# Optimization experiments

Hardware: AMD Instinct MI355X
Metric: run time of the kernel (lower is better)

## Reference

```python
import jax, jax.numpy as jnp
import numpy as np

DICE_W, BCE_W = 1.0, 1.0
BBOX_W = 0.025
L1_W, GIOU_W = 1.0, 1.0  # assumed BoxLoss weighting: loss = l1.sum(-1) + (1 - giou)


def _xywh_to_xyxy(b):
    cx, cy, w, h = b[..., 0], b[..., 1], b[..., 2], b[..., 3]
    return jnp.stack([cx - w / 2, cy - h / 2, cx + w / 2, cy + h / 2], axis=-1)


def _xyxy_to_xywh(b):
    x1, y1, x2, y2 = b[..., 0], b[..., 1], b[..., 2], b[..., 3]
    return jnp.stack([(x1 + x2) / 2, (y1 + y2) / 2, x2 - x1, y2 - y1], axis=-1)


def _giou(a, b):
    # a, b: [N,4] xyxy, paired GIoU
    ix1 = jnp.maximum(a[:, 0], b[:, 0]); iy1 = jnp.maximum(a[:, 1], b[:, 1])
    ix2 = jnp.minimum(a[:, 2], b[:, 2]); iy2 = jnp.minimum(a[:, 3], b[:, 3])
    inter = jnp.clip(ix2 - ix1, 0) * jnp.clip(iy2 - iy1, 0)
    area_a = jnp.clip(a[:, 2] - a[:, 0], 0) * jnp.clip(a[:, 3] - a[:, 1], 0)
    area_b = jnp.clip(b[:, 2] - b[:, 0], 0) * jnp.clip(b[:, 3] - b[:, 1], 0)
    union = area_a + area_b - inter
    iou = inter / jnp.maximum(union, 1e-6)
    cx1 = jnp.minimum(a[:, 0], b[:, 0]); cy1 = jnp.minimum(a[:, 1], b[:, 1])
    cx2 = jnp.maximum(a[:, 2], b[:, 2]); cy2 = jnp.maximum(a[:, 3], b[:, 3])
    c = jnp.clip(cx2 - cx1, 0) * jnp.clip(cy2 - cy1, 0)
    return iou - (c - union) / jnp.maximum(c, 1e-6)


def _box_loss_per_sample(pred_xywh, tgt_xywh):
    l1 = jnp.abs(pred_xywh - tgt_xywh).sum(-1)
    g = 1.0 - _giou(_xywh_to_xyxy(pred_xywh), _xywh_to_xyxy(tgt_xywh))
    return L1_W * l1 + GIOU_W * g


def _forward(pred_mask, pred_bbox, gt_bbox_rand, target_mask, img_h, img_w):
    B = pred_mask.shape[0]
    H, W = img_h, img_w
    tgt = target_mask.astype(pred_mask.dtype)          # [B,H,W] binary
    logits = pred_mask[:, 0]                           # [B,H,W]
    probs = jax.nn.sigmoid(logits)

    # ---- seg_loss: dice + bce (both mean-reduced) ----
    p = probs.reshape(B, -1); t = tgt.reshape(B, -1)
    dice = 1.0 - (2.0 * (p * t).sum(1) + 1.0) / (p.sum(1) + t.sum(1) + 1.0)
    x = logits.reshape(B, -1)
    bce = jnp.maximum(x, 0) - x * t + jnp.log1p(jnp.exp(-jnp.abs(x)))
    loss_mask = DICE_W * dice.mean() + BCE_W * bce.mean()

    # ---- bbox_loss: gt x1y1x2y2 (pixels) -> normalized cxcywh ----
    gx1 = gt_bbox_rand[:, 0] * (0.45 * W); gy1 = gt_bbox_rand[:, 1] * (0.45 * H)
    gx2 = gx1 + 1.0 + gt_bbox_rand[:, 2] * (0.5 * W)
    gy2 = gy1 + 1.0 + gt_bbox_rand[:, 3] * (0.5 * H)
    gt_xyxy = jnp.stack([gx1, gy1, gx2, gy2], axis=-1)
    # original divides by img_size [H,W] repeated -> [H,W,H,W] (square imgs)
    norm_div = jnp.asarray([H, W, H, W], dtype=pred_bbox.dtype)
    gt_norm = _xyxy_to_xywh(gt_xyxy) / norm_div
    loss_det = _box_loss_per_sample(pred_bbox, gt_norm).mean() * BBOX_W

    # ---- boxseg_iouloss2 (vectorized over the per-batch python loop) ----
    box_xyxy = _xywh_to_xyxy(pred_bbox)                # normalized xyxy
    scale = jnp.asarray([W, H, W, H], dtype=pred_bbox.dtype)
    pix = (box_xyxy * scale).astype(jnp.int32)         # trunc like .to(int)
    x1p = jnp.clip(pix[:, 0], 0, W); x2p = jnp.clip(pix[:, 2], 0, W)
    y1p = jnp.clip(pix[:, 1], 0, H); y2p = jnp.clip(pix[:, 3], 0, H)
    seg_bin = (probs > 0.5).astype(pred_mask.dtype)    # S2Bthr == B2Sthr == 0.5
    xs = jnp.arange(W); ys = jnp.arange(H)
    in_x = (xs[None, :] >= x1p[:, None]) & (xs[None, :] < x2p[:, None])  # [B,W]
    in_y = (ys[None, :] >= y1p[:, None]) & (ys[None, :] < y2p[:, None])  # [B,H]
    inside = in_y[:, :, None] & in_x[:, None, :]                          # [B,H,W]
    inter = (seg_bin * inside).sum((1, 2))
    area = seg_bin.sum((1, 2))
    s2b_iou = jnp.where(area > 0, inter / jnp.maximum(area, 1.0), 0.0)
    loss_s2b = (1.0 - s2b_iou).mean()

    # get_maskouterbox: per-sample min/max of coords where mask is on
    mb = seg_bin.astype(bool)
    x1o = jnp.min(jnp.where(mb, xs[None, None, :], W), axis=(1, 2))
    y1o = jnp.min(jnp.where(mb, ys[None, :, None], H), axis=(1, 2))
    x2o = jnp.max(jnp.where(mb, xs[None, None, :], -1), axis=(1, 2))
    y2o = jnp.max(jnp.where(mb, ys[None, :, None], -1), axis=(1, 2))
    present = (area > 0)[:, None]
    outer = jnp.stack([x1o, y1o, x2o, y2o], axis=-1).astype(pred_bbox.dtype)
    outer = jnp.where(present, outer, 0.0) / scale
    loss_b2s = _box_loss_per_sample(_xyxy_to_xywh(outer), _xyxy_to_xywh(box_xyxy)).mean()

    return loss_mask + loss_det + loss_s2b + loss_b2s


def setup_inputs() -> dict:
    key = jax.random.key(0)
    k1, k2, k3, k4 = jax.random.split(key, 4)
    B, H, W = 64, 512, 512
    return {
        "pred_mask": jax.random.normal(k1, (B, 1, H, W), dtype=jnp.float32),
        "pred_bbox": jax.random.uniform(k2, (B, 4), dtype=jnp.float32),
        "gt_bbox_rand": jax.random.uniform(k3, (B, 4), dtype=jnp.float32),
        "target_mask": jax.random.randint(k4, (B, H, W), 0, 2, dtype=jnp.int32),
        "img_h": H,
        "img_w": W,
    }


def reference(pred_mask, pred_bbox, gt_bbox_rand, target_mask, img_h, img_w):
    return _forward(pred_mask, pred_bbox, gt_bbox_rand, target_mask, img_h, img_w)
```

## Files before the change

### kernel.cpp

```cpp
#include <hip/hip_runtime.h>
#include <math.h>


#define TPB 256

__device__ inline float box_loss_xywh(const float pb[4], const float tb[4]) {
    float l1 = fabsf(pb[0] - tb[0]) + fabsf(pb[1] - tb[1]) +
               fabsf(pb[2] - tb[2]) + fabsf(pb[3] - tb[3]);
    float ax1 = pb[0] - 0.5f * pb[2], ay1 = pb[1] - 0.5f * pb[3];
    float ax2 = pb[0] + 0.5f * pb[2], ay2 = pb[1] + 0.5f * pb[3];
    float bx1 = tb[0] - 0.5f * tb[2], by1 = tb[1] - 0.5f * tb[3];
    float bx2 = tb[0] + 0.5f * tb[2], by2 = tb[1] + 0.5f * tb[3];

    float ix1 = fmaxf(ax1, bx1), iy1 = fmaxf(ay1, by1);
    float ix2 = fminf(ax2, bx2), iy2 = fminf(ay2, by2);
    float inter  = fmaxf(ix2 - ix1, 0.f) * fmaxf(iy2 - iy1, 0.f);
    float area_a = fmaxf(ax2 - ax1, 0.f) * fmaxf(ay2 - ay1, 0.f);
    float area_b = fmaxf(bx2 - bx1, 0.f) * fmaxf(by2 - by1, 0.f);
    float uni = area_a + area_b - inter;
    float iou = inter / fmaxf(uni, 1e-6f);
    float cx1 = fminf(ax1, bx1), cy1 = fminf(ay1, by1);
    float cx2 = fmaxf(ax2, bx2), cy2 = fmaxf(ay2, by2);
    float c = fmaxf(cx2 - cx1, 0.f) * fmaxf(cy2 - cy1, 0.f);
    float giou = iou - (c - uni) / fmaxf(c, 1e-6f);
    return l1 + (1.0f - giou);
}

struct Acc {
    float s_pt, s_p, s_bce;
    int c_t, c_area, c_inter;
    unsigned rmask, colmask;
};

__device__ __forceinline__ void proc4(const float4 xv, const int4 tv,
                                      int yloc, int ybase, int by1, int by2,
                                      int inx0, int inx1, int inx2, int inx3,
                                      Acc& a)
{
    float xs[4] = {xv.x, xv.y, xv.z, xv.w};
    int   ts[4] = {tv.x, tv.y, tv.z, tv.w};
    int pos[4];
    #pragma unroll
    for (int j = 0; j < 4; ++j) {
        float xl = xs[j];
        bool  t  = ts[j] != 0;
        float e  = __expf(-fabsf(xl));
        float r  = __builtin_amdgcn_rcpf(1.f + e);
        float p  = (xl >= 0.f) ? r : e * r;
        a.s_bce += fmaxf(xl, 0.f) - (t ? xl : 0.f) - __logf(r);
        a.s_p   += p;
        a.s_pt  += t ? p : 0.f;
        a.c_t   += ts[j];
        pos[j] = xl > 0.f;
    }
    int anyp = pos[0] | pos[1] | pos[2] | pos[3];
    a.c_area  += pos[0] + pos[1] + pos[2] + pos[3];
    a.colmask |= (unsigned)(pos[0] | (pos[1] << 1) | (pos[2] << 2) | (pos[3] << 3));
    a.rmask   |= (unsigned)anyp << yloc;
    const int y = ybase + yloc;
    const int inrow = (y >= by1) & (y < by2);
    a.c_inter += inrow ? ((pos[0] & inx0) + (pos[1] & inx1) +
                          (pos[2] & inx2) + (pos[3] & inx3)) : 0;
}

__global__ __launch_bounds__(TPB, 8)
void uh_reduce(const float* __restrict__ pred_mask,
               const int*   __restrict__ target_mask,
               const float* __restrict__ pred_bbox,
               const int*   __restrict__ pH, const int* __restrict__ pW,
               float* __restrict__ wf, int* __restrict__ wi,
               int HW, int N)
{
    const int b      = blockIdx.y;
    const int chunk  = blockIdx.x;
    const int nchunk = gridDim.x;
    const int W = *pW;
    const int H = *pH;

    float c0 = pred_bbox[b * 4 + 0], c1 = pred_bbox[b * 4 + 1];
    float c2 = pred_bbox[b * 4 + 2], c3 = pred_bbox[b * 4 + 3];
    const int bx1 = min(max((int)((c0 - 0.5f * c2) * (float)W), 0), W);
    const int by1 = min(max((int)((c1 - 0.5f * c3) * (float)H), 0), H);
    const int bx2 = min(max((int)((c0 + 0.5f * c2) * (float)W), 0), W);
    const int by2 = min(max((int)((c1 + 0.5f * c3) * (float)H), 0), H);

    const int chunk_px = HW / nchunk;
    const int rows     = chunk_px / W;
    const int tpr      = W >> 2;
    const int rpi      = TPB / tpr;
    const int iters    = rows / rpi;
    const int rowoff   = threadIdx.x / tpr;
    const int cx       = (threadIdx.x - rowoff * tpr) << 2;
    const int ybase    = chunk * rows;

    const int inx0 = (cx + 0 >= bx1) & (cx + 0 < bx2);
    const int inx1 = (cx + 1 >= bx1) & (cx + 1 < bx2);
    const int inx2 = (cx + 2 >= bx1) & (cx + 2 < bx2);
    const int inx3 = (cx + 3 >= bx1) & (cx + 3 < bx2);

    const long boff = (long)b * HW + (long)(ybase + rowoff) * W + cx;
    const float* pp = pred_mask + boff;
    const int*   tp = target_mask + boff;
    const int    stride = rpi * W;

    Acc a = {0.f, 0.f, 0.f, 0, 0, 0, 0u, 0u};
    int yloc = rowoff;

    const int npairs = iters >> 1;
    float4 xa0 = *(const float4*)pp;
    int4   ta0 = *(const int4*)tp;
    float4 xa1 = *(const float4*)(pp + stride);
    int4   ta1 = *(const int4*)(tp + stride);
    pp += 2 * stride; tp += 2 * stride;

    for (int g = 0; g < npairs - 1; ++g) {
        float4 xb0 = *(const float4*)pp;
        int4   tb0 = *(const int4*)tp;
        float4 xb1 = *(const float4*)(pp + stride);
        int4   tb1 = *(const int4*)(tp + stride);
        pp += 2 * stride; tp += 2 * stride;

        proc4(xa0, ta0, yloc,       ybase, by1, by2, inx0, inx1, inx2, inx3, a);
        proc4(xa1, ta1, yloc + rpi, ybase, by1, by2, inx0, inx1, inx2, inx3, a);
        yloc += 2 * rpi;

        xa0 = xb0; ta0 = tb0; xa1 = xb1; ta1 = tb1;
    }
    proc4(xa0, ta0, yloc,       ybase, by1, by2, inx0, inx1, inx2, inx3, a);
    proc4(xa1, ta1, yloc + rpi, ybase, by1, by2, inx0, inx1, inx2, inx3, a);

    int xmn = W, xmx = -1, ymn = H, ymx = -1;
    if (a.colmask) {
        xmn = cx + (__ffs(a.colmask) - 1);
        xmx = cx + (31 - __clz(a.colmask));
    }
    if (a.rmask) {
        ymn = ybase + (__ffs(a.rmask) - 1);
        ymx = ybase + (31 - __clz(a.rmask));
    }

    float s_pt = a.s_pt, s_p = a.s_p, s_bce = a.s_bce;
    int c_t = a.c_t, c_area = a.c_area, c_inter = a.c_inter;
    #pragma unroll
    for (int o = 32; o; o >>= 1) {
        s_pt  += __shfl_down(s_pt,  o, 64);
        s_p   += __shfl_down(s_p,   o, 64);
        s_bce += __shfl_down(s_bce, o, 64);
        c_t    += __shfl_down(c_t,    o, 64);
        c_area += __shfl_down(c_area, o, 64);
        c_inter+= __shfl_down(c_inter,o, 64);
        xmn = min(xmn, __shfl_down(xmn, o, 64));
        ymn = min(ymn, __shfl_down(ymn, o, 64));
        xmx = max(xmx, __shfl_down(xmx, o, 64));
        ymx = max(ymx, __shfl_down(ymx, o, 64));
    }

    __shared__ float smf[3][4];
    __shared__ int   smi[7][4];
    const int wid = threadIdx.x >> 6;
    if ((threadIdx.x & 63) == 0) {
        smf[0][wid] = s_pt;  smf[1][wid] = s_p;  smf[2][wid] = s_bce;
        smi[0][wid] = c_t;   smi[1][wid] = c_area; smi[2][wid] = c_inter;
        smi[3][wid] = xmn;   smi[4][wid] = ymn;
        smi[5][wid] = xmx;   smi[6][wid] = ymx;
    }
    __syncthreads();
    if (threadIdx.x == 0) {
        float a0 = 0.f, a1 = 0.f, a2 = 0.f;
        int i0 = 0, i1 = 0, i2 = 0;
        int m3 = W, m4 = H, m5 = -1, m6 = -1;
        #pragma unroll
        for (int w = 0; w < 4; ++w) {
            a0 += smf[0][w]; a1 += smf[1][w]; a2 += smf[2][w];
            i0 += smi[0][w]; i1 += smi[1][w]; i2 += smi[2][w];
            m3 = min(m3, smi[3][w]); m4 = min(m4, smi[4][w]);
            m5 = max(m5, smi[5][w]); m6 = max(m6, smi[6][w]);
        }
        const int idx = b * nchunk + chunk;
        wf[0 * N + idx] = a0; wf[1 * N + idx] = a1; wf[2 * N + idx] = a2;
        wi[0 * N + idx] = i0; wi[1 * N + idx] = i1; wi[2 * N + idx] = i2;
        wi[3 * N + idx] = m3; wi[4 * N + idx] = m4;
        wi[5 * N + idx] = m5; wi[6 * N + idx] = m6;
    }
}

__global__ __launch_bounds__(TPB)
void uh_final(const float* __restrict__ pred_bbox,
              const float* __restrict__ gt_bbox,
              const int* __restrict__ pH, const int* __restrict__ pW,
              const float* __restrict__ wf, const int* __restrict__ wi,
              int B, int HW, int nchunk, float* __restrict__ out)
{
    const int W = *pW, H = *pH;
    const int N = B * nchunk;
    const int tid = threadIdx.x;
    const int b   = tid >> 2;
    const int q   = tid & 3;

    float v = 0.f;
    if (b < B) {
        float s_pt = 0.f, s_p = 0.f, s_bce = 0.f;
        int c_t = 0, c_area = 0, c_inter = 0;
        int xmn = W, ymn = H, xmx = -1, ymx = -1;
        for (int c = q; c < nchunk; c += 4) {
            const int idx = b * nchunk + c;
            s_pt  += wf[0 * N + idx];
            s_p   += wf[1 * N + idx];
            s_bce += wf[2 * N + idx];
            c_t    += wi[0 * N + idx];
            c_area += wi[1 * N + idx];
            c_inter+= wi[2 * N + idx];
            xmn = min(xmn, wi[3 * N + idx]); ymn = min(ymn, wi[4 * N + idx]);
            xmx = max(xmx, wi[5 * N + idx]); ymx = max(ymx, wi[6 * N + idx]);
        }
        #pragma unroll
        for (int o = 1; o < 4; o <<= 1) {
            s_pt  += __shfl_xor(s_pt,  o, 64);
            s_p   += __shfl_xor(s_p,   o, 64);
            s_bce += __shfl_xor(s_bce, o, 64);
            c_t    += __shfl_xor(c_t,    o, 64);
            c_area += __shfl_xor(c_area, o, 64);
            c_inter+= __shfl_xor(c_inter,o, 64);
            xmn = min(xmn, __shfl_xor(xmn, o, 64));
            ymn = min(ymn, __shfl_xor(ymn, o, 64));
            xmx = max(xmx, __shfl_xor(xmx, o, 64));
            ymx = max(ymx, __shfl_xor(ymx, o, 64));
        }

        if (q == 0) {
            float dice = 1.f - (2.f * s_pt + 1.f) / (s_p + (float)c_t + 1.f);

            float pb[4] = {pred_bbox[b*4+0], pred_bbox[b*4+1],
                           pred_bbox[b*4+2], pred_bbox[b*4+3]};
            float g0 = gt_bbox[b*4+0], g1 = gt_bbox[b*4+1];
            float g2 = gt_bbox[b*4+2], g3 = gt_bbox[b*4+3];
            float gx1 = g0 * (0.45f * (float)W);
            float gy1 = g1 * (0.45f * (float)H);
            float gx2 = gx1 + 1.0f + g2 * (0.5f * (float)W);
            float gy2 = gy1 + 1.0f + g3 * (0.5f * (float)H);
            float gt[4] = { ((gx1 + gx2) * 0.5f) / (float)H,
                            ((gy1 + gy2) * 0.5f) / (float)W,
                            (gx2 - gx1) / (float)H,
                            (gy2 - gy1) / (float)W };
            float det = 0.025f * box_loss_xywh(pb, gt);

            float iou_s2b = (c_area > 0)
                              ? (float)c_inter / fmaxf((float)c_area, 1.f) : 0.f;
            float s2b = 1.f - iou_s2b;

            float ox1, oy1, ox2, oy2;
            if (c_area > 0) {
                ox1 = (float)xmn; oy1 = (float)ymn;
                ox2 = (float)xmx; oy2 = (float)ymx;
            } else {
                ox1 = oy1 = ox2 = oy2 = 0.f;
            }
            ox1 /= (float)W; ox2 /= (float)W;
            oy1 /= (float)H; oy2 /= (float)H;
            float ow[4] = { (ox1 + ox2) * 0.5f, (oy1 + oy2) * 0.5f,
                            ox2 - ox1, oy2 - oy1 };
            float px1 = pb[0] - 0.5f * pb[2], py1 = pb[1] - 0.5f * pb[3];
            float px2 = pb[0] + 0.5f * pb[2], py2 = pb[1] + 0.5f * pb[3];
            float pw[4] = { (px1 + px2) * 0.5f, (py1 + py2) * 0.5f,
                            px2 - px1, py2 - py1 };
            float b2s = box_loss_xywh(ow, pw);

            v = dice + s_bce / (float)HW + det + s2b + b2s;
        }
    }

    #pragma unroll
    for (int o = 32; o; o >>= 1) v += __shfl_down(v, o, 64);
    __shared__ float sv[4];
    if ((tid & 63) == 0) sv[tid >> 6] = v;
    __syncthreads();
    if (tid == 0) out[0] = (sv[0] + sv[1] + sv[2] + sv[3]) / (float)B;
}

extern "C" void kernel_launch(void* const* d_in, const int* in_sizes, int n_in,
                              void* d_out, int out_size, void* d_ws, size_t ws_size,
                              hipStream_t stream) {
    const float* pred_mask   = (const float*)d_in[0];
    const float* pred_bbox   = (const float*)d_in[1];
    const float* gt_bbox     = (const float*)d_in[2];
    const int*   target_mask = (const int*)d_in[3];
    const int*   pH          = (const int*)d_in[4];
    const int*   pW          = (const int*)d_in[5];
    float* out = (float*)d_out;

    const int B  = in_sizes[1] / 4;
    const int HW = in_sizes[0] / B;

    int bps = 32;
    if ((size_t)10 * sizeof(int) * B * bps > ws_size) bps = 16;
    const int N = B * bps;

    float* wf = (float*)d_ws;
    int*   wi = (int*)d_ws + (size_t)3 * N;

    dim3 grid(bps, B);
    uh_reduce<<<grid, TPB, 0, stream>>>(pred_mask, target_mask, pred_bbox,
                                        pH, pW, wf, wi, HW, N);
    uh_final<<<1, TPB, 0, stream>>>(pred_bbox, gt_bbox, pH, pW, wf, wi,
                                    B, HW, bps, out);
}
```

Before: 159.5 us.

## Process eight columns per thread with four-row batches and cheaper BCE math

Each thread now covers 8 contiguous columns instead of 4 and loads four rows per iteration (16 vector loads in flight) in place of the software-pipelined pair loop. The BCE term is split into a relu accumulator plus a log2 sum scaled once at the end, and sigmoid uses 1-r instead of e*r. Column and row masks are built as bitmasks reduced with popcount, and the row mask now indexes iteration number rather than the local row. The launch-bounds occupancy hint is dropped, which may raise register use and lower occupancy. The intent is more memory-level parallelism and fewer ALU ops per pixel.

```diff
diff --git a/kernel.cpp b/kernel.cpp
--- a/kernel.cpp
+++ b/kernel.cpp
@@ -26,44 +26,7 @@
     return l1 + (1.0f - giou);
 }
 
-struct Acc {
-    float s_pt, s_p, s_bce;
-    int c_t, c_area, c_inter;
-    unsigned rmask, colmask;
-};
-
-__device__ __forceinline__ void proc4(const float4 xv, const int4 tv,
-                                      int yloc, int ybase, int by1, int by2,
-                                      int inx0, int inx1, int inx2, int inx3,
-                                      Acc& a)
-{
-    float xs[4] = {xv.x, xv.y, xv.z, xv.w};
-    int   ts[4] = {tv.x, tv.y, tv.z, tv.w};
-    int pos[4];
-    #pragma unroll
-    for (int j = 0; j < 4; ++j) {
-        float xl = xs[j];
-        bool  t  = ts[j] != 0;
-        float e  = __expf(-fabsf(xl));
-        float r  = __builtin_amdgcn_rcpf(1.f + e);
-        float p  = (xl >= 0.f) ? r : e * r;
-        a.s_bce += fmaxf(xl, 0.f) - (t ? xl : 0.f) - __logf(r);
-        a.s_p   += p;
-        a.s_pt  += t ? p : 0.f;
-        a.c_t   += ts[j];
-        pos[j] = xl > 0.f;
-    }
-    int anyp = pos[0] | pos[1] | pos[2] | pos[3];
-    a.c_area  += pos[0] + pos[1] + pos[2] + pos[3];
-    a.colmask |= (unsigned)(pos[0] | (pos[1] << 1) | (pos[2] << 2) | (pos[3] << 3));
-    a.rmask   |= (unsigned)anyp << yloc;
-    const int y = ybase + yloc;
-    const int inrow = (y >= by1) & (y < by2);
-    a.c_inter += inrow ? ((pos[0] & inx0) + (pos[1] & inx1) +
-                          (pos[2] & inx2) + (pos[3] & inx3)) : 0;
-}
-
-__global__ __launch_bounds__(TPB, 8)
+__global__ __launch_bounds__(TPB)
 void uh_reduce(const float* __restrict__ pred_mask,
                const int*   __restrict__ target_mask,
                const float* __restrict__ pred_bbox,
@@ -86,61 +49,93 @@
 
     const int chunk_px = HW / nchunk;
     const int rows     = chunk_px / W;
-    const int tpr      = W >> 2;
+    const int tpr      = W >> 3;
     const int rpi      = TPB / tpr;
     const int iters    = rows / rpi;
     const int rowoff   = threadIdx.x / tpr;
-    const int cx       = (threadIdx.x - rowoff * tpr) << 2;
+    const int cx       = (threadIdx.x - rowoff * tpr) << 3;
     const int ybase    = chunk * rows;
 
-    const int inx0 = (cx + 0 >= bx1) & (cx + 0 < bx2);
-    const int inx1 = (cx + 1 >= bx1) & (cx + 1 < bx2);
-    const int inx2 = (cx + 2 >= bx1) & (cx + 2 < bx2);
-    const int inx3 = (cx + 3 >= bx1) & (cx + 3 < bx2);
+    unsigned inxmask = 0;
+    #pragma unroll
+    for (int j = 0; j < 8; ++j)
+        inxmask |= (unsigned)((cx + j >= bx1) & (cx + j < bx2)) << j;
 
     const long boff = (long)b * HW + (long)(ybase + rowoff) * W + cx;
     const float* pp = pred_mask + boff;
     const int*   tp = target_mask + boff;
     const int    stride = rpi * W;
 
-    Acc a = {0.f, 0.f, 0.f, 0, 0, 0, 0u, 0u};
-    int yloc = rowoff;
-
-    const int npairs = iters >> 1;
-    float4 xa0 = *(const float4*)pp;
-    int4   ta0 = *(const int4*)tp;
-    float4 xa1 = *(const float4*)(pp + stride);
-    int4   ta1 = *(const int4*)(tp + stride);
-    pp += 2 * stride; tp += 2 * stride;
-
-    for (int g = 0; g < npairs - 1; ++g) {
-        float4 xb0 = *(const float4*)pp;
-        int4   tb0 = *(const int4*)tp;
-        float4 xb1 = *(const float4*)(pp + stride);
-        int4   tb1 = *(const int4*)(tp + stride);
-        pp += 2 * stride; tp += 2 * stride;
-
-        proc4(xa0, ta0, yloc,       ybase, by1, by2, inx0, inx1, inx2, inx3, a);
-        proc4(xa1, ta1, yloc + rpi, ybase, by1, by2, inx0, inx1, inx2, inx3, a);
-        yloc += 2 * rpi;
-
-        xa0 = xb0; ta0 = tb0; xa1 = xb1; ta1 = tb1;
-    }
-    proc4(xa0, ta0, yloc,       ybase, by1, by2, inx0, inx1, inx2, inx3, a);
-    proc4(xa1, ta1, yloc + rpi, ybase, by1, by2, inx0, inx1, inx2, inx3, a);
+    float s_pt = 0.f, s_p = 0.f, slg2 = 0.f, s_relu = 0.f;
+    int c_t = 0, c_area = 0, c_inter = 0;
+    unsigned rmask = 0, colmask = 0;
+
+    for (int gb = 0; gb < iters; gb += 4) {
+        float4 xa0 = *(const float4*)(pp);
+        float4 xb0 = *(const float4*)(pp + 4);
+        int4   ta0 = *(const int4*)(tp);
+        int4   tb0 = *(const int4*)(tp + 4);
+        float4 xa1 = *(const float4*)(pp + stride);
+        float4 xb1 = *(const float4*)(pp + stride + 4);
+        int4   ta1 = *(const int4*)(tp + stride);
+        int4   tb1 = *(const int4*)(tp + stride + 4);
+        float4 xa2 = *(const float4*)(pp + 2 * stride);
+        float4 xb2 = *(const float4*)(pp + 2 * stride + 4);
+        int4   ta2 = *(const int4*)(tp + 2 * stride);
+        int4   tb2 = *(const int4*)(tp + 2 * stride + 4);
+        float4 xa3 = *(const float4*)(pp + 3 * stride);
+        float4 xb3 = *(const float4*)(pp + 3 * stride + 4);
+        int4   ta3 = *(const int4*)(tp + 3 * stride);
+        int4   tb3 = *(const int4*)(tp + 3 * stride + 4);
+        pp += 4 * stride; tp += 4 * stride;
+
+        #define PROC_ROW(G, XA, XB, TA, TB)                                   \
+        {                                                                     \
+            const float xs[8] = {XA.x, XA.y, XA.z, XA.w,                      \
+                                 XB.x, XB.y, XB.z, XB.w};                     \
+            const int   ts[8] = {TA.x, TA.y, TA.z, TA.w,                      \
+                                 TB.x, TB.y, TB.z, TB.w};                     \
+            unsigned m8 = 0;                                                  \
+            _Pragma("unroll")                                                 \
+            for (int j = 0; j < 8; ++j) {                                     \
+                float xl = xs[j];                                             \
+                bool  t  = ts[j] != 0;                                        \
+                float e  = __expf(-fabsf(xl));           \
+                float r  = __builtin_amdgcn_rcpf(1.f + e);                    \
+                slg2    += __log2f(r);                  \
+                float p  = (xl >= 0.f) ? r : 1.f - r;                         \
+                s_p     += p;                                                 \
+                s_pt    += t ? p : 0.f;                                       \
+                s_relu  += fmaxf(t ? -xl : xl, 0.f);                          \
+                c_t     += ts[j];                                             \
+                m8      |= (unsigned)(xl > 0.f) << j;                         \
+            }                                                                 \
+            c_area  += __popc(m8);                                            \
+            const int y = ybase + rowoff + (G) * rpi;                         \
+            c_inter += ((y >= by1) & (y < by2)) ? __popc(m8 & inxmask) : 0;   \
+            colmask |= m8;                                                    \
+            rmask   |= (m8 ? 1u : 0u) << (G);                                 \
+        }
+
+        PROC_ROW(gb + 0, xa0, xb0, ta0, tb0)
+        PROC_ROW(gb + 1, xa1, xb1, ta1, tb1)
+        PROC_ROW(gb + 2, xa2, xb2, ta2, tb2)
+        PROC_ROW(gb + 3, xa3, xb3, ta3, tb3)
+        #undef PROC_ROW
+    }
+
+    float s_bce = fmaf(-0.69314718055994531f, slg2, s_relu);
 
     int xmn = W, xmx = -1, ymn = H, ymx = -1;
-    if (a.colmask) {
-        xmn = cx + (__ffs(a.colmask) - 1);
-        xmx = cx + (31 - __clz(a.colmask));
-    }
-    if (a.rmask) {
-        ymn = ybase + (__ffs(a.rmask) - 1);
-        ymx = ybase + (31 - __clz(a.rmask));
-    }
-
-    float s_pt = a.s_pt, s_p = a.s_p, s_bce = a.s_bce;
-    int c_t = a.c_t, c_area = a.c_area, c_inter = a.c_inter;
+    if (colmask) {
+        xmn = cx + (__ffs(colmask) - 1);
+        xmx = cx + (31 - __clz(colmask));
+    }
+    if (rmask) {
+        ymn = ybase + rowoff + (__ffs(rmask) - 1) * rpi;
+        ymx = ybase + rowoff + (31 - __clz(rmask)) * rpi;
+    }
+
     #pragma unroll
     for (int o = 32; o; o >>= 1) {
         s_pt  += __shfl_down(s_pt,  o, 64);
```

Result: no change. 159.6 us (+0.1%).
